# Kernel optimization log

Hardware: AMD Instinct MI355X
Metric: run time of the kernel (lower is better)

The kernel has to match this reference:

```python
import jax, jax.numpy as jnp
import numpy as np

COLUMN_COUNT = 2048
CELLS_PER_COLUMN = 32
NUM_CELLS = COLUMN_COUNT * CELLS_PER_COLUMN
MAX_SEGMENTS = 16
MAX_SYNAPSES = 32
ACTIVATION_THRESHOLD = 13
PERMANENCE_CONNECTED = 0.5


def setup_inputs() -> dict:
    key = jax.random.key(0)
    k1, k2, k3, k4, k5 = jax.random.split(key, 5)
    active_columns = jax.random.randint(k1, (COLUMN_COUNT,), 0, 2).astype(jnp.float32)
    prev_active = jax.random.randint(k2, (NUM_CELLS,), 0, 2).astype(jnp.float32)
    prev_predictive = jax.random.randint(k3, (NUM_CELLS,), 0, 2).astype(jnp.float32)
    seg_pre = jax.random.randint(k4, (NUM_CELLS, MAX_SEGMENTS, MAX_SYNAPSES), 0, NUM_CELLS, dtype=jnp.int32)
    seg_perm = jax.random.uniform(k5, (NUM_CELLS, MAX_SEGMENTS, MAX_SYNAPSES), dtype=jnp.float32)
    return {
        'active_columns': active_columns,
        'prev_active': prev_active,
        'prev_predictive': prev_predictive,
        'seg_pre': seg_pre,
        'seg_perm': seg_perm,
    }


def _best_segment_activity(seg_pre, connected, active_vec):
    """Per cell: max over segments of (# synapses that are connected AND whose
    presynaptic cell is active). Mirrors _get_segment_activity/_get_best_matching_segment."""
    pre_active = active_vec[seg_pre] > 0          # [N, S, K] irregular gather
    counts = jnp.sum(connected & pre_active, axis=-1)  # [N, S]
    return jnp.max(counts, axis=-1)               # [N]


def reference(active_columns, prev_active, prev_predictive, seg_pre, seg_perm):
    C, cpc = COLUMN_COUNT, CELLS_PER_COLUMN
    connected = seg_perm >= PERMANENCE_CONNECTED   # [N, S, K]

    col_active = active_columns > 0                           # [C]
    pred = (prev_predictive > 0).reshape(C, cpc)              # [C, cpc]
    col_has_pred = jnp.any(pred, axis=1)                      # [C]

    # Active cells: predicted cells if any prediction in column, else burst (all cells).
    new_active = jnp.where(col_active[:, None],
                           jnp.where(col_has_pred[:, None], pred, True),
                           False)                             # [C, cpc]
    active_flat = new_active.reshape(-1).astype(jnp.float32)  # [N]

    # New predictive cells: any segment with activity >= activation_threshold
    # w.r.t. the NEW active set.
    best_act = _best_segment_activity(seg_pre, connected, active_flat)  # [N]
    new_predictive = (best_act >= ACTIVATION_THRESHOLD).astype(jnp.float32)

    # Anomaly: fraction of active columns with no predicted cell.
    n_active_cols = jnp.sum(col_active)
    n_predicted = jnp.sum(col_active & col_has_pred)
    anomaly = (1.0 - n_predicted / jnp.maximum(n_active_cols, 1)).astype(jnp.float32)

    return active_flat, new_predictive, anomaly


if __name__ == '__main__':
    out = reference(**setup_inputs())
    print([o.shape for o in out])
```

## Files before the change

kernel.cpp:

```cpp
#include <hip/hip_runtime.h>

#define COLS    2048
#define CPC     32
#define NCELLS  65536
#define SEGS    16
#define SYN     32
#define THRESH  13

#define CPB     8
#define PREDICT_GRID (NCELLS / CPB)

__global__ __launch_bounds__(256) void tm_active_kernel(
    const float* __restrict__ active_columns,
    const float* __restrict__ prev_predictive,
    float* __restrict__ out_active,
    unsigned int* __restrict__ ws_mask,
    unsigned char* __restrict__ ws_flags)
{
    int n = blockIdx.x * 256 + threadIdx.x;
    int c = n >> 5;
    int j = n & 31;
    int lane = threadIdx.x & 63;

    bool predbit    = prev_predictive[n] > 0.0f;
    bool col_active = active_columns[c] > 0.0f;

    unsigned long long pb = __ballot(predbit);
    unsigned int colmask = (lane < 32) ? (unsigned int)pb : (unsigned int)(pb >> 32);
    bool has_pred = (colmask != 0u);

    bool active = col_active && (has_pred ? predbit : true);
    out_active[n] = active ? 1.0f : 0.0f;

    unsigned long long ab = __ballot(active);
    if (lane == 0)  ws_mask[c] = (unsigned int)ab;
    if (lane == 32) ws_mask[c] = (unsigned int)(ab >> 32);

    if (j == 0)
        ws_flags[c] = (unsigned char)((col_active ? 1 : 0) |
                                      ((col_active && has_pred) ? 2 : 0));
}

typedef const __attribute__((address_space(1))) void* gas_ptr;
typedef __attribute__((address_space(3)))       void* las_ptr;

__device__ __forceinline__ void dma_1kb(const char* g, char* lds, int lane) {
    __builtin_amdgcn_global_load_lds((gas_ptr)(g + lane * 16), (las_ptr)lds, 16, 0, 0);
}

__global__ __launch_bounds__(256) void tm_predict_kernel(
    const int*   __restrict__ seg_pre,
    const float* __restrict__ seg_perm,
    const unsigned int* __restrict__ ws_mask,
    const unsigned char* __restrict__ ws_flags,
    float* __restrict__ out_pred,
    float* __restrict__ out_anomaly)
{
    __shared__ unsigned int mask[COLS];
    __shared__ char pre_lds [CPB * 2048];
    __shared__ char perm_lds[CPB * 2048];

    int tid  = threadIdx.x;
    int wave = tid >> 6;
    int lane = tid & 63;
    int cell0 = blockIdx.x * CPB;

    #pragma unroll
    for (int k = 0; k < 2; ++k) {
        int c = 2 * wave + k;
        const char* gp = (const char*)(seg_pre  + (size_t)(cell0 + c) * 512);
        const char* gq = (const char*)(seg_perm + (size_t)(cell0 + c) * 512);
        dma_1kb(gp,        pre_lds  + c * 2048,        lane);
        dma_1kb(gp + 1024, pre_lds  + c * 2048 + 1024, lane);
        dma_1kb(gq,        perm_lds + c * 2048,        lane);
        dma_1kb(gq + 1024, perm_lds + c * 2048 + 1024, lane);
    }

    #pragma unroll
    for (int i = 0; i < 2; ++i)
        ((uint4*)mask)[tid + 256 * i] = ((const uint4*)ws_mask)[tid + 256 * i];

    __syncthreads();

    #pragma unroll
    for (int k = 0; k < 2; ++k) {
        int c = 2 * wave + k;
        const int4*   pl = (const int4*)  (pre_lds  + c * 2048);
        const float4* ql = (const float4*)(perm_lds + c * 2048);

        int4   p0 = pl[lane], p1 = pl[lane + 64];
        float4 q0 = ql[lane], q1 = ql[lane + 64];

        int c0 = 0, c1 = 0;
        c0 += (q0.x >= 0.5f && ((mask[(unsigned)p0.x >> 5] >> ((unsigned)p0.x & 31u)) & 1u)) ? 1 : 0;
        c0 += (q0.y >= 0.5f && ((mask[(unsigned)p0.y >> 5] >> ((unsigned)p0.y & 31u)) & 1u)) ? 1 : 0;
        c0 += (q0.z >= 0.5f && ((mask[(unsigned)p0.z >> 5] >> ((unsigned)p0.z & 31u)) & 1u)) ? 1 : 0;
        c0 += (q0.w >= 0.5f && ((mask[(unsigned)p0.w >> 5] >> ((unsigned)p0.w & 31u)) & 1u)) ? 1 : 0;
        c1 += (q1.x >= 0.5f && ((mask[(unsigned)p1.x >> 5] >> ((unsigned)p1.x & 31u)) & 1u)) ? 1 : 0;
        c1 += (q1.y >= 0.5f && ((mask[(unsigned)p1.y >> 5] >> ((unsigned)p1.y & 31u)) & 1u)) ? 1 : 0;
        c1 += (q1.z >= 0.5f && ((mask[(unsigned)p1.z >> 5] >> ((unsigned)p1.z & 31u)) & 1u)) ? 1 : 0;
        c1 += (q1.w >= 0.5f && ((mask[(unsigned)p1.w >> 5] >> ((unsigned)p1.w & 31u)) & 1u)) ? 1 : 0;

        int v = c0 | (c1 << 16);
        v += __shfl_xor(v, 1, 64);
        v += __shfl_xor(v, 2, 64);
        v += __shfl_xor(v, 4, 64);
        int m = max(v & 0xffff, v >> 16);
        m = max(m, __shfl_xor(m, 8, 64));
        m = max(m, __shfl_xor(m, 16, 64));
        m = max(m, __shfl_xor(m, 32, 64));

        if (lane == 0)
            out_pred[cell0 + c] = (m >= THRESH) ? 1.0f : 0.0f;
    }

    if (blockIdx.x == 0 && tid < 64) {
        const unsigned int* f = (const unsigned int*)ws_flags;
        int na = 0, np = 0;
        #pragma unroll
        for (int i = 0; i < 8; ++i) {
            unsigned w = f[tid * 8 + i];
            na += __popc(w & 0x01010101u);
            np += __popc(w & 0x02020202u);
        }
        int v = na | (np << 16);
        v += __shfl_xor(v, 1, 64);
        v += __shfl_xor(v, 2, 64);
        v += __shfl_xor(v, 4, 64);
        v += __shfl_xor(v, 8, 64);
        v += __shfl_xor(v, 16, 64);
        v += __shfl_xor(v, 32, 64);
        if (tid == 0) {
            int NA = v & 0xffff, NP = v >> 16;
            *out_anomaly = 1.0f - (float)NP / (float)(NA > 1 ? NA : 1);
        }
    }
}

extern "C" void kernel_launch(void* const* d_in, const int* in_sizes, int n_in,
                              void* d_out, int out_size, void* d_ws, size_t ws_size,
                              hipStream_t stream) {
    const float* active_columns  = (const float*)d_in[0];
    const float* prev_predictive = (const float*)d_in[2];
    const int*   seg_pre         = (const int*)d_in[3];
    const float* seg_perm        = (const float*)d_in[4];
    float* out = (float*)d_out;

    unsigned int*  ws_mask  = (unsigned int*)d_ws;
    unsigned char* ws_flags = (unsigned char*)d_ws + COLS * sizeof(unsigned int);

    tm_active_kernel<<<NCELLS / 256, 256, 0, stream>>>(
        active_columns, prev_predictive, out, ws_mask, ws_flags);

    tm_predict_kernel<<<PREDICT_GRID, 256, 0, stream>>>(
        seg_pre, seg_perm, ws_mask, ws_flags,
        out + NCELLS, out + 2 * NCELLS);
}
```

Measured before the change: 285.5 us.

## Double-buffer per-wave LDS staging of segment data over 16 cells per wave

Each wave now handles 16 cells instead of 2, using a two-slot LDS buffer. It issues the async global-to-LDS DMA for the next cell while computing on the current one, with explicit vmcnt and lgkmcnt waits. Predictions are packed into a bitmask and written once per wave at the end. This cuts the grid 8x, which amortises the 8 KB mask load per block and overlaps memory latency with compute. The cost is fewer blocks and less memory-level parallelism per wave, and correctness depends on the hand-written waitcnt ordering.

```diff
diff --git a/kernel.cpp b/kernel.cpp
--- a/kernel.cpp
+++ b/kernel.cpp
@@ -7,7 +7,8 @@
 #define SYN     32
 #define THRESH  13
 
-#define CPB     8
+#define CPW     16
+#define CPB     (4 * CPW)
 #define PREDICT_GRID (NCELLS / CPB)
 
 __global__ __launch_bounds__(256) void tm_active_kernel(
@@ -57,36 +58,50 @@
     float* __restrict__ out_anomaly)
 {
     __shared__ unsigned int mask[COLS];
-    __shared__ char pre_lds [CPB * 2048];
-    __shared__ char perm_lds[CPB * 2048];
+    __shared__ char stage[4][2][4096];
 
     int tid  = threadIdx.x;
     int wave = tid >> 6;
     int lane = tid & 63;
-    int cell0 = blockIdx.x * CPB;
+    int base = blockIdx.x * CPB + wave * CPW;
 
-    #pragma unroll
-    for (int k = 0; k < 2; ++k) {
-        int c = 2 * wave + k;
-        const char* gp = (const char*)(seg_pre  + (size_t)(cell0 + c) * 512);
-        const char* gq = (const char*)(seg_perm + (size_t)(cell0 + c) * 512);
-        dma_1kb(gp,        pre_lds  + c * 2048,        lane);
-        dma_1kb(gp + 1024, pre_lds  + c * 2048 + 1024, lane);
-        dma_1kb(gq,        perm_lds + c * 2048,        lane);
-        dma_1kb(gq + 1024, perm_lds + c * 2048 + 1024, lane);
+    {
+        const char* gp = (const char*)(seg_pre  + (size_t)base * 512);
+        const char* gq = (const char*)(seg_perm + (size_t)base * 512);
+        char* L = stage[wave][0];
+        dma_1kb(gp,        L,        lane);
+        dma_1kb(gp + 1024, L + 1024, lane);
+        dma_1kb(gq,        L + 2048, lane);
+        dma_1kb(gq + 1024, L + 3072, lane);
     }
 
-    #pragma unroll
-    for (int i = 0; i < 2; ++i)
-        ((uint4*)mask)[tid + 256 * i] = ((const uint4*)ws_mask)[tid + 256 * i];
+    ((uint4*)mask)[tid]       = ((const uint4*)ws_mask)[tid];
+    ((uint4*)mask)[tid + 256] = ((const uint4*)ws_mask)[tid + 256];
 
     __syncthreads();
 
+    unsigned pmask = 0;
     #pragma unroll
-    for (int k = 0; k < 2; ++k) {
-        int c = 2 * wave + k;
-        const int4*   pl = (const int4*)  (pre_lds  + c * 2048);
-        const float4* ql = (const float4*)(perm_lds + c * 2048);
+    for (int i = 0; i < CPW; ++i) {
+        char* L = stage[wave][i & 1];
+
+        if (i + 1 < CPW) {
+            asm volatile("s_waitcnt lgkmcnt(0)" ::: "memory");
+            const char* gp = (const char*)(seg_pre  + (size_t)(base + i + 1) * 512);
+            const char* gq = (const char*)(seg_perm + (size_t)(base + i + 1) * 512);
+            char* Ln = stage[wave][(i + 1) & 1];
+            dma_1kb(gp,        Ln,        lane);
+            dma_1kb(gp + 1024, Ln + 1024, lane);
+            dma_1kb(gq,        Ln + 2048, lane);
+            dma_1kb(gq + 1024, Ln + 3072, lane);
+            __builtin_amdgcn_sched_barrier(0);
+            asm volatile("s_waitcnt vmcnt(4)" ::: "memory");
+        } else {
+            asm volatile("s_waitcnt vmcnt(0)" ::: "memory");
+        }
+
+        const int4*   pl = (const int4*)  L;
+        const float4* ql = (const float4*)(L + 2048);
 
         int4   p0 = pl[lane], p1 = pl[lane + 64];
         float4 q0 = ql[lane], q1 = ql[lane + 64];
@@ -110,9 +125,11 @@
         m = max(m, __shfl_xor(m, 16, 64));
         m = max(m, __shfl_xor(m, 32, 64));
 
-        if (lane == 0)
-            out_pred[cell0 + c] = (m >= THRESH) ? 1.0f : 0.0f;
+        pmask |= (m >= THRESH) ? (1u << i) : 0u;
     }
+
+    if (lane < CPW)
+        out_pred[base + lane] = ((pmask >> lane) & 1u) ? 1.0f : 0.0f;
 
     if (blockIdx.x == 0 && tid < 64) {
         const unsigned int* f = (const unsigned int*)ws_flags;
```

After: 287.1 us. Within noise of the previous version (+0.6%).
